# Optimization experiments

Measured on AMD Instinct MI355X. Metric: run time of the kernel, lower is better.

Reference implementation:

```python
import jax, jax.numpy as jnp
import numpy as np

B = 4096        # batch_size
D = 256         # feature_dim
N = 9000000     # dataset size (state buffer length)
G = 100         # num_groups
ALPHA = 0.5     # alpha_weight
GAMMA = 0.8
RHO = 8.0
LAM = 1.0       # lambada
ETA_P = 0.01
EPS = 1e-14
CLIP = 5.0


def setup_inputs() -> dict:
    key = jax.random.key(0)
    k = jax.random.split(key, 6)
    zis = jax.random.normal(k[0], (B, D), jnp.float32)
    zjs = jax.random.normal(k[1], (B, D), jnp.float32)
    # per-sample learned temperatures, small positive values
    taus_I = 0.01 + 0.2 * jax.random.uniform(k[2], (N,), jnp.float32)
    taus_T = 0.01 + 0.2 * jax.random.uniform(k[3], (N,), jnp.float32)
    group_info_I = jax.random.randint(k[4], (N,), 0, G, dtype=jnp.int32)
    group_info_T = jax.random.randint(k[5], (N,), 0, G, dtype=jnp.int32)
    ids = jnp.arange(B, dtype=jnp.int32)  # unique sample indices
    zeros_N = jnp.zeros((N,), jnp.float32)
    return {
        "zis": zis, "zjs": zjs,
        "s_I": zeros_N, "s_T": zeros_N, "b_I": zeros_N, "b_T": zeros_N,
        "z_I": jnp.zeros((G,), jnp.float32), "z_T": jnp.zeros((G,), jnp.float32),
        "p_I": jnp.ones((G,), jnp.float32) / G, "p_T": jnp.ones((G,), jnp.float32) / G,
        "taus_I": taus_I, "taus_T": taus_T,
        "ids": ids, "group_info_I": group_info_I, "group_info_T": group_info_T,
    }


def _l2norm(x):
    return x / jnp.maximum(jnp.linalg.norm(x, axis=1, keepdims=True), 1e-12)


def reference(zis, zjs, s_I, s_T, b_I, b_T, z_I, z_T, p_I, p_T,
              taus_I, taus_T, ids, group_info_I, group_info_T):
    zis = _l2norm(zis)
    zjs = _l2norm(zjs)
    sim = zis @ zjs.T                                   # [B, B]
    diag = jnp.diagonal(sim)                            # [B]
    mask_neg = 1.0 - jnp.eye(B, dtype=sim.dtype)
    image_diffs = sim - diag[:, None]
    text_diffs = sim - diag[None, :]

    tau_I = taus_I[ids]                                 # [B]
    tau_T = taus_T[ids]
    idt = jax.lax.stop_gradient(image_diffs / tau_I[:, None])
    tdt = jax.lax.stop_gradient(text_diffs / tau_T[None, :])

    # running max state (numerically-stable exp)
    old_b_I = b_I[ids]
    b_I_new = jnp.maximum(jnp.max(idt, axis=1), old_b_I)    # [B]
    old_b_T = b_T[ids]
    b_T_new = jnp.maximum(jnp.max(tdt, axis=0), old_b_T)    # [B]
    b_I = b_I.at[ids].set(b_I_new)
    b_T = b_T.at[ids].set(b_T_new)

    exp_I = jnp.exp(idt - b_I_new[:, None]) * mask_neg
    exp_T = jnp.exp(tdt - b_T_new[None, :]) * mask_neg
    g_I = jnp.sum(exp_I, axis=1)                         # [B]
    g_T = jnp.sum(exp_T, axis=0)                         # [B]

    # EMA of softmax denominators with max-rescaling
    s_I_new = (1.0 - GAMMA) * s_I[ids] * jnp.exp(old_b_I - b_I_new) + GAMMA * g_I
    s_T_new = (1.0 - GAMMA) * s_T[ids] * jnp.exp(old_b_T - b_T_new) + GAMMA * g_T
    s_I = s_I.at[ids].set(s_I_new)
    s_T = s_T.at[ids].set(s_T_new)
    s_I_c = jnp.maximum(s_I_new, EPS)
    s_T_c = jnp.maximum(s_T_new, EPS)

    w_I = exp_I / s_I_c[:, None]
    w_T = exp_T / s_T_c[None, :]

    gid_I = group_info_I[ids]                            # [B]
    gid_T = group_info_T[ids]
    gw_I = G * p_I[gid_I]                                # [B]
    gw_T = G * p_T[gid_T]

    image_loss = jnp.sum(w_I * gw_I[:, None] * image_diffs, axis=1)   # [B]
    text_loss = jnp.sum(w_T * gw_T[None, :] * text_diffs, axis=0)     # [B]
    total_loss = ALPHA * image_loss.mean() + (1.0 - ALPHA) * text_loss.mean()

    # per-group adversarial weight update
    F_I = tau_I * (jnp.log(s_I_c) + b_I_new + RHO)       # [B]
    F_T = tau_T * (jnp.log(s_T_c) + b_T_new + RHO)
    ones_b = jnp.ones((B,), sim.dtype)
    cnt_I = jnp.maximum(jax.ops.segment_sum(ones_b, gid_I, num_segments=G), 1.0)
    cnt_T = jnp.maximum(jax.ops.segment_sum(ones_b, gid_T, num_segments=G), 1.0)
    grad_p_I = jax.ops.segment_sum(F_I, gid_I, num_segments=G) / cnt_I
    grad_p_T = jax.ops.segment_sum(F_T, gid_T, num_segments=G) / cnt_T

    z_I = (1.0 - GAMMA) * z_I + GAMMA * grad_p_I
    z_T = (1.0 - GAMMA) * z_T + GAMMA * grad_p_T
    grad_hp_I = -LAM * jnp.log(p_I + EPS) - LAM
    grad_hp_T = -LAM * jnp.log(p_T + EPS) - LAM
    new_p_I = p_I * jnp.exp(2.0 * ETA_P * jnp.clip(z_I + grad_hp_I, -CLIP, CLIP))
    new_p_T = p_T * jnp.exp(2.0 * ETA_P * jnp.clip(z_T + grad_hp_T, -CLIP, CLIP))
    p_I = new_p_I / new_p_I.sum()
    p_T = new_p_T / new_p_T.sum()

    return total_loss, p_I, p_T
```

## Files before the change

kernel.cpp:

```cpp
#include <hip/hip_runtime.h>
#include <hip/hip_bf16.h>
#include <math.h>

#define BB 4096
#define DD 256
#define GG 100
#define GAMMA_C 0.8f
#define RHO_C 8.0f
#define ALPHA_C 0.5f
#define EPS_C 1e-14f
#define NSR 64
#define NSC 128

typedef __bf16 bf16x8 __attribute__((ext_vector_type(8)));
typedef float f32x16 __attribute__((ext_vector_type(16)));

__device__ inline int swzLoc(int r31, int k) {
    return ((k >> 4) << 9) | (((((k >> 3) & 1) << 5) | r31) << 3) | (k & 7);
}

__device__ inline float blockReduceSum(float v, float* lds) {
    for (int o = 32; o > 0; o >>= 1) v += __shfl_down(v, o);
    int lane = threadIdx.x & 63, wid = threadIdx.x >> 6;
    if (lane == 0) lds[wid] = v;
    __syncthreads();
    if (threadIdx.x == 0) {
        float r = lds[0];
        int nw = blockDim.x >> 6;
        for (int w = 1; w < nw; w++) r += lds[w];
        lds[0] = r;
    }
    __syncthreads();
    float r = lds[0];
    __syncthreads();
    return r;
}

__global__ void __launch_bounds__(256) norm_kernel(const float* __restrict__ zis,
                            const float* __restrict__ zjs,
                            ushort* __restrict__ zhi, ushort* __restrict__ zlo,
                            ushort* __restrict__ whi, ushort* __restrict__ wlo,
                            float* __restrict__ diag, float* __restrict__ acc) {
    __shared__ ushort st[4][8192];
    int rb = blockIdx.x;
    int wv = threadIdx.x >> 6, lane = threadIdx.x & 63;
    if (rb == 0) { acc[threadIdx.x] = 0.f; acc[threadIdx.x + 256] = 0.f; }
    for (int rr = 0; rr < 8; rr++) {
        int r = rb * 32 + wv * 8 + rr;
        float4 zv = *(const float4*)&zis[r * DD + lane * 4];
        float4 wv4 = *(const float4*)&zjs[r * DD + lane * 4];
        float sz = zv.x * zv.x + zv.y * zv.y + zv.z * zv.z + zv.w * zv.w;
        float sw = wv4.x * wv4.x + wv4.y * wv4.y + wv4.z * wv4.z + wv4.w * wv4.w;
        float dt = zv.x * wv4.x + zv.y * wv4.y + zv.z * wv4.z + zv.w * wv4.w;
        for (int mask = 1; mask <= 32; mask <<= 1) {
            sz += __shfl_xor(sz, mask);
            sw += __shfl_xor(sw, mask);
            dt += __shfl_xor(dt, mask);
        }
        float iz = 1.0f / fmaxf(sqrtf(sz), 1e-12f);
        float iw = 1.0f / fmaxf(sqrtf(sw), 1e-12f);
        if (lane == 0) diag[r] = dt * iz * iw;
        float nz[4] = {zv.x * iz, zv.y * iz, zv.z * iz, zv.w * iz};
        float nw[4] = {wv4.x * iw, wv4.y * iw, wv4.z * iw, wv4.w * iw};
        int r31 = wv * 8 + rr;
        for (int e = 0; e < 4; e++) {
            int k = lane * 4 + e;
            int li = swzLoc(r31, k);
            __hip_bfloat16 hz = __float2bfloat16(nz[e]);
            __hip_bfloat16 lz = __float2bfloat16(nz[e] - __bfloat162float(hz));
            __hip_bfloat16 hw = __float2bfloat16(nw[e]);
            __hip_bfloat16 lw = __float2bfloat16(nw[e] - __bfloat162float(hw));
            st[0][li] = *(ushort*)&hz;
            st[1][li] = *(ushort*)&lz;
            st[2][li] = *(ushort*)&hw;
            st[3][li] = *(ushort*)&lw;
        }
    }
    __syncthreads();
    size_t base = (size_t)rb * 8192;
    ushort* dsts[4] = {zhi + base, zlo + base, whi + base, wlo + base};
    for (int a = 0; a < 4; a++) {
        uint4* d = (uint4*)dsts[a];
        const uint4* s = (const uint4*)st[a];
        for (int it = 0; it < 4; it++) {
            int idx = it * 256 + threadIdx.x;
            d[idx] = s[idx];
        }
    }
}

__global__ void __launch_bounds__(256, 4) fused_tile(const ushort* __restrict__ Ahi,
        const ushort* __restrict__ Alo, const ushort* __restrict__ Bhi,
        const ushort* __restrict__ Blo, const float* __restrict__ diag,
        const float* __restrict__ tausI, const float* __restrict__ tausT,
        const int* __restrict__ ids,
        float* __restrict__ pmR, float* __restrict__ pgR, float* __restrict__ pwR,
        float* __restrict__ pmC, float* __restrict__ pgC, float* __restrict__ pwC) {
    __shared__ float rDiag[128], rITau[128];
    __shared__ float cDiag[64], cITau[64];

    int lane = threadIdx.x & 63;
    int wv = threadIdx.x >> 6;
    int bm = blockIdx.y * 128, bn = blockIdx.x * 64;
    int h = lane >> 5, cl = lane & 31;

    if (threadIdx.x < 128) {
        int r = bm + threadIdx.x;
        rDiag[threadIdx.x] = diag[r];
        rITau[threadIdx.x] = 1.0f / tausI[ids[r]];
    } else if (threadIdx.x < 192) {
        int c = bn + threadIdx.x - 128;
        cDiag[threadIdx.x - 128] = diag[c];
        cITau[threadIdx.x - 128] = 1.0f / tausT[ids[c]];
    }

    int aBase = (blockIdx.y * 4 + wv) * 8192;
    int b0 = (blockIdx.x * 2) * 8192;
    int b1 = b0 + 8192;
    int lofs = lane * 8;

    f32x16 acc[2] = {};
    bf16x8 ah, al, bh0, bl0, bh1, bl1;
    ah  = *(const bf16x8*)&Ahi[aBase + lofs];
    al  = *(const bf16x8*)&Alo[aBase + lofs];
    bh0 = *(const bf16x8*)&Bhi[b0 + lofs];
    bl0 = *(const bf16x8*)&Blo[b0 + lofs];
    bh1 = *(const bf16x8*)&Bhi[b1 + lofs];
    bl1 = *(const bf16x8*)&Blo[b1 + lofs];
#pragma unroll
    for (int s = 0; s < 16; s++) {
        bf16x8 nah, nal, nbh0, nbl0, nbh1, nbl1;
        if (s < 15) {
            int so = (s + 1) * 512 + lofs;
            nah  = *(const bf16x8*)&Ahi[aBase + so];
            nal  = *(const bf16x8*)&Alo[aBase + so];
            nbh0 = *(const bf16x8*)&Bhi[b0 + so];
            nbl0 = *(const bf16x8*)&Blo[b0 + so];
            nbh1 = *(const bf16x8*)&Bhi[b1 + so];
            nbl1 = *(const bf16x8*)&Blo[b1 + so];
        }
        acc[0] = __builtin_amdgcn_mfma_f32_32x32x16_bf16(ah, bh0, acc[0], 0, 0, 0);
        acc[0] = __builtin_amdgcn_mfma_f32_32x32x16_bf16(ah, bl0, acc[0], 0, 0, 0);
        acc[0] = __builtin_amdgcn_mfma_f32_32x32x16_bf16(al, bh0, acc[0], 0, 0, 0);
        acc[1] = __builtin_amdgcn_mfma_f32_32x32x16_bf16(ah, bh1, acc[1], 0, 0, 0);
        acc[1] = __builtin_amdgcn_mfma_f32_32x32x16_bf16(ah, bl1, acc[1], 0, 0, 0);
        acc[1] = __builtin_amdgcn_mfma_f32_32x32x16_bf16(al, bh1, acc[1], 0, 0, 0);
        ah = nah; al = nal; bh0 = nbh0; bl0 = nbl0; bh1 = nbh1; bl1 = nbl1;
    }
    __syncthreads();

    float cd2[2], cit2[2], cbloc[2], cg[2] = {}, cw[2] = {};
    for (int u = 0; u < 2; u++) {
        int clc = u * 32 + cl;
        cd2[u] = cDiag[clc];
        cit2[u] = cITau[clc];
        float m = -INFINITY;
        for (int reg = 0; reg < 16; reg++) m = fmaxf(m, acc[u][reg]);
        m = fmaxf(m, __shfl_xor(m, 32));
        cbloc[u] = (m - cd2[u]) * cit2[u];
    }
    for (int u = 0; u < 2; u++) {
        int gc = bn + u * 32 + cl;
        for (int reg = 0; reg < 16; reg++) {
            int gr = bm + wv * 32 + (reg & 3) + 4 * h + 8 * (reg >> 2);
            float v = acc[u][reg];
            bool off = gr != gc;
            float dvT = v - cd2[u];
            float eT = off ? __expf(dvT * cit2[u] - cbloc[u]) : 0.f;
            cg[u] += eT;
            cw[u] += eT * dvT;
        }
    }
    int stripeC = blockIdx.y * 4 + wv;
    for (int u = 0; u < 2; u++) {
        cg[u] += __shfl_xor(cg[u], 32);
        cw[u] += __shfl_xor(cw[u], 32);
        if (h == 0) {
            size_t o = (size_t)stripeC * BB + bn + u * 32 + cl;
            pmC[o] = cbloc[u];
            pgC[o] = cg[u];
            pwC[o] = cw[u];
        }
    }

    int stripeR = blockIdx.x;
    for (int q = 0; q < 4; q++) {
        float rd4[4], rit4[4], bloc[4], rg[4] = {}, rw[4] = {};
        for (int j = 0; j < 4; j++) {
            int rl = wv * 32 + 8 * q + 4 * h + j;
            rd4[j] = rDiag[rl];
            rit4[j] = rITau[rl];
        }
        for (int j = 0; j < 4; j++) {
            float m = fmaxf(acc[0][4 * q + j], acc[1][4 * q + j]);
            for (int mask = 1; mask <= 16; mask <<= 1)
                m = fmaxf(m, __shfl_xor(m, mask));
            bloc[j] = (m - rd4[j]) * rit4[j];
        }
        for (int u = 0; u < 2; u++) {
            int gc = bn + u * 32 + cl;
            for (int j = 0; j < 4; j++) {
                int gr = bm + wv * 32 + 8 * q + 4 * h + j;
                float v = acc[u][4 * q + j];
                bool off = gr != gc;
                float dvI = v - rd4[j];
                float eI = off ? __expf(dvI * rit4[j] - bloc[j]) : 0.f;
                rg[j] += eI;
                rw[j] += eI * dvI;
            }
        }
        for (int j = 0; j < 4; j++)
            for (int mask = 1; mask <= 16; mask <<= 1) {
                rg[j] += __shfl_xor(rg[j], mask);
                rw[j] += __shfl_xor(rw[j], mask);
            }
        if (cl == 0) {
            size_t o = (size_t)stripeR * BB + bm + wv * 32 + 8 * q + 4 * h;
            *(float4*)&pmR[o] = make_float4(bloc[0], bloc[1], bloc[2], bloc[3]);
            *(float4*)&pgR[o] = make_float4(rg[0], rg[1], rg[2], rg[3]);
            *(float4*)&pwR[o] = make_float4(rw[0], rw[1], rw[2], rw[3]);
        }
    }
}

__global__ void __launch_bounds__(256) fin_kernel(
        const float* __restrict__ pmR, const float* __restrict__ pgR,
        const float* __restrict__ pwR, const float* __restrict__ pmC,
        const float* __restrict__ pgC, const float* __restrict__ pwC,
        const float* __restrict__ sI, const float* __restrict__ bI,
        const float* __restrict__ tausI, const int* __restrict__ gInfI,
        const float* __restrict__ pI,
        const float* __restrict__ sT, const float* __restrict__ bT,
        const float* __restrict__ tausT, const int* __restrict__ gInfT,
        const float* __restrict__ pT,
        const int* __restrict__ ids, float* __restrict__ acc,
        const float* __restrict__ zI, const float* __restrict__ zT,
        float* __restrict__ out) {
    __shared__ float lds[8];
    __shared__ float binF[GG], binC[GG];
    __shared__ int lastFlag;
    if (threadIdx.x < GG) { binF[threadIdx.x] = 0.f; binC[threadIdx.x] = 0.f; }
    __syncthreads();
    int side = blockIdx.x >> 4;
    int i = (blockIdx.x & 15) * 256 + threadIdx.x;
    int ns = side ? NSC : NSR;
    const float* pm = side ? pmC : pmR;
    const float* pg = side ? pgC : pgR;
    const float* pw = side ? pwC : pwR;
    const float* sS = side ? sT : sI;
    const float* bS = side ? bT : bI;
    const float* taus = side ? tausT : tausI;
    const int* ginfo = side ? gInfT : gInfI;
    const float* pP = side ? pT : pI;

    int id = ids[i];
    float oldb = bS[id];
    float m = -INFINITY;
    for (int s = 0; s < ns; s++) m = fmaxf(m, pm[(size_t)s * BB + i]);
    float bfin = fmaxf(m, oldb);
    float g = 0.f, wsum = 0.f;
    for (int s = 0; s < ns; s++) {
        float f = __expf(pm[(size_t)s * BB + i] - bfin);
        g += pg[(size_t)s * BB + i] * f;
        wsum += pw[(size_t)s * BB + i] * f;
    }
    float tau = taus[id];
    float snew = (1.f - GAMMA_C) * sS[id] * expf(oldb - bfin) + GAMMA_C * g;
    float sc = fmaxf(snew, EPS_C);
    int gid = ginfo[id];
    float gw = (float)GG * pP[gid];
    float loss = gw * wsum / sc;
    float F = tau * (logf(sc) + bfin + RHO_C);
    atomicAdd(&binF[gid], F);
    atomicAdd(&binC[gid], 1.0f);
    float lsum = blockReduceSum(loss, lds);
    if (threadIdx.x == 0) atomicAdd(&acc[side], lsum);
    __syncthreads();
    if (threadIdx.x < GG) {
        atomicAdd(&acc[2 + side * 200 + threadIdx.x], binF[threadIdx.x]);
        atomicAdd(&acc[102 + side * 200 + threadIdx.x], binC[threadIdx.x]);
    }

    __threadfence();
    if (threadIdx.x == 0) {
        int old = atomicAdd((int*)&acc[408], 1);
        lastFlag = (old == 31);
    }
    __syncthreads();
    if (!lastFlag) return;

    int gg = threadIdx.x;
    float npI = 0.f, npT = 0.f;
    if (gg < GG) {
        float cI = __hip_atomic_load(&acc[102 + gg], __ATOMIC_RELAXED, __HIP_MEMORY_SCOPE_AGENT);
        float fI = __hip_atomic_load(&acc[2 + gg], __ATOMIC_RELAXED, __HIP_MEMORY_SCOPE_AGENT);
        float gpI = fI / fmaxf(cI, 1.f);
        float zi = (1.f - GAMMA_C) * zI[gg] + GAMMA_C * gpI;
        float ghpI = -logf(pI[gg] + EPS_C) - 1.f;
        float ti = fminf(fmaxf(zi + ghpI, -5.f), 5.f);
        npI = pI[gg] * expf(0.02f * ti);

        float cT = __hip_atomic_load(&acc[302 + gg], __ATOMIC_RELAXED, __HIP_MEMORY_SCOPE_AGENT);
        float fT = __hip_atomic_load(&acc[202 + gg], __ATOMIC_RELAXED, __HIP_MEMORY_SCOPE_AGENT);
        float gpT = fT / fmaxf(cT, 1.f);
        float zt = (1.f - GAMMA_C) * zT[gg] + GAMMA_C * gpT;
        float ghpT = -logf(pT[gg] + EPS_C) - 1.f;
        float tt = fminf(fmaxf(zt + ghpT, -5.f), 5.f);
        npT = pT[gg] * expf(0.02f * tt);
    }
    float sumI = blockReduceSum(npI, lds);
    float sumT = blockReduceSum(npT, lds);
    if (gg < GG) {
        out[1 + gg] = npI / sumI;
        out[101 + gg] = npT / sumT;
    }
    if (gg == 0) {
        float lI = __hip_atomic_load(&acc[0], __ATOMIC_RELAXED, __HIP_MEMORY_SCOPE_AGENT);
        float lT = __hip_atomic_load(&acc[1], __ATOMIC_RELAXED, __HIP_MEMORY_SCOPE_AGENT);
        out[0] = ALPHA_C * (lI / (float)BB) + (1.f - ALPHA_C) * (lT / (float)BB);
    }
}

extern "C" void kernel_launch(void* const* d_in, const int* in_sizes, int n_in,
                              void* d_out, int out_size, void* d_ws, size_t ws_size,
                              hipStream_t stream) {
    const float* zis   = (const float*)d_in[0];
    const float* zjs   = (const float*)d_in[1];
    const float* s_I   = (const float*)d_in[2];
    const float* s_T   = (const float*)d_in[3];
    const float* b_I   = (const float*)d_in[4];
    const float* b_T   = (const float*)d_in[5];
    const float* z_I   = (const float*)d_in[6];
    const float* z_T   = (const float*)d_in[7];
    const float* p_I   = (const float*)d_in[8];
    const float* p_T   = (const float*)d_in[9];
    const float* tausI = (const float*)d_in[10];
    const float* tausT = (const float*)d_in[11];
    const int*   ids   = (const int*)d_in[12];
    const int*   gInfI = (const int*)d_in[13];
    const int*   gInfT = (const int*)d_in[14];
    float* out = (float*)d_out;

    char* ws = (char*)d_ws;
    ushort* zhi = (ushort*)ws;
    ushort* zlo = zhi + (size_t)BB * DD;
    ushort* whi = zlo + (size_t)BB * DD;
    ushort* wlo = whi + (size_t)BB * DD;
    float* acc  = (float*)(wlo + (size_t)BB * DD);
    float* diag = acc + 512;
    float* pmR  = diag + BB;
    float* pgR  = pmR + (size_t)NSR * BB;
    float* pwR  = pgR + (size_t)NSR * BB;
    float* pmC  = pwR + (size_t)NSR * BB;
    float* pgC  = pmC + (size_t)NSC * BB;
    float* pwC  = pgC + (size_t)NSC * BB;

    norm_kernel<<<128, 256, 0, stream>>>(zis, zjs, zhi, zlo, whi, wlo, diag, acc);
    fused_tile<<<dim3(64, 32), 256, 0, stream>>>(zhi, zlo, whi, wlo, diag,
            tausI, tausT, ids, pmR, pgR, pwR, pmC, pgC, pwC);
    fin_kernel<<<32, 256, 0, stream>>>(pmR, pgR, pwR, pmC, pgC, pwC,
            s_I, b_I, tausI, gInfI, p_I, s_T, b_T, tausT, gInfT, p_T, ids, acc,
            z_I, z_T, out);
}
```

Measured before the change: 325.1 us.

## Merge column partials in-block and parallelize final reduction across more blocks

The tile kernel now merges its four per-wave column partials (max, exp-sum, weighted sum) through shared memory before writing, which cuts the column-side partial buffer from 128 stripes to 32. The finalize kernel is relaunched with 128 blocks, each splitting the stripe loop over four thread groups with an online log-sum-exp merge, followed by a shared-memory combine. Both changes target the latency of the serial 64/128-iteration reduction done by only 32 blocks. In exchange the tile kernel gains an extra __syncthreads and some shared-memory use, which could affect occupancy.

Result: faster. 279.5 us (-14.0%).

```diff
diff --git a/kernel.cpp b/kernel.cpp
--- a/kernel.cpp
+++ b/kernel.cpp
@@ -10,7 +10,7 @@
 #define ALPHA_C 0.5f
 #define EPS_C 1e-14f
 #define NSR 64
-#define NSC 128
+#define NSC 32
 
 typedef __bf16 bf16x8 __attribute__((ext_vector_type(8)));
 typedef float f32x16 __attribute__((ext_vector_type(16)));
@@ -98,6 +98,7 @@
         float* __restrict__ pmC, float* __restrict__ pgC, float* __restrict__ pwC) {
     __shared__ float rDiag[128], rITau[128];
     __shared__ float cDiag[64], cITau[64];
+    __shared__ float cmS[4][64], cgS[4][64], cwS[4][64];
 
     int lane = threadIdx.x & 63;
     int wv = threadIdx.x >> 6;
@@ -171,16 +172,29 @@
             cw[u] += eT * dvT;
         }
     }
-    int stripeC = blockIdx.y * 4 + wv;
     for (int u = 0; u < 2; u++) {
         cg[u] += __shfl_xor(cg[u], 32);
         cw[u] += __shfl_xor(cw[u], 32);
         if (h == 0) {
-            size_t o = (size_t)stripeC * BB + bn + u * 32 + cl;
-            pmC[o] = cbloc[u];
-            pgC[o] = cg[u];
-            pwC[o] = cw[u];
-        }
+            cmS[wv][u * 32 + cl] = cbloc[u];
+            cgS[wv][u * 32 + cl] = cg[u];
+            cwS[wv][u * 32 + cl] = cw[u];
+        }
+    }
+    __syncthreads();
+    if (threadIdx.x < 64) {
+        int c = threadIdx.x;
+        float m = fmaxf(fmaxf(cmS[0][c], cmS[1][c]), fmaxf(cmS[2][c], cmS[3][c]));
+        float g = 0.f, w = 0.f;
+        for (int wq = 0; wq < 4; wq++) {
+            float f = __expf(cmS[wq][c] - m);
+            g += cgS[wq][c] * f;
+            w += cwS[wq][c] * f;
+        }
+        size_t o = (size_t)blockIdx.y * BB + bn + c;
+        pmC[o] = m;
+        pgC[o] = g;
+        pwC[o] = w;
     }
 
     int stripeR = blockIdx.x;
@@ -238,11 +252,14 @@
         float* __restrict__ out) {
     __shared__ float lds[8];
     __shared__ float binF[GG], binC[GG];
+    __shared__ float mS[4][64], gS[4][64], wS[4][64];
     __shared__ int lastFlag;
     if (threadIdx.x < GG) { binF[threadIdx.x] = 0.f; binC[threadIdx.x] = 0.f; }
-    __syncthreads();
-    int side = blockIdx.x >> 4;
-    int i = (blockIdx.x & 15) * 256 + threadIdx.x;
+    int side = blockIdx.x >> 6;
+    int chunk = blockIdx.x & 63;
+    int il = threadIdx.x & 63;
+    int sg = threadIdx.x >> 6;
+    int i = chunk * 64 + il;
     int ns = side ? NSC : NSR;
     const float* pm = side ? pmC : pmR;
     const float* pg = side ? pgC : pgR;
@@ -253,26 +270,45 @@
     const int* ginfo = side ? gInfT : gInfI;
     const float* pP = side ? pT : pI;
 
-    int id = ids[i];
-    float oldb = bS[id];
-    float m = -INFINITY;
-    for (int s = 0; s < ns; s++) m = fmaxf(m, pm[(size_t)s * BB + i]);
-    float bfin = fmaxf(m, oldb);
-    float g = 0.f, wsum = 0.f;
-    for (int s = 0; s < ns; s++) {
-        float f = __expf(pm[(size_t)s * BB + i] - bfin);
-        g += pg[(size_t)s * BB + i] * f;
-        wsum += pw[(size_t)s * BB + i] * f;
-    }
-    float tau = taus[id];
-    float snew = (1.f - GAMMA_C) * sS[id] * expf(oldb - bfin) + GAMMA_C * g;
-    float sc = fmaxf(snew, EPS_C);
-    int gid = ginfo[id];
-    float gw = (float)GG * pP[gid];
-    float loss = gw * wsum / sc;
-    float F = tau * (logf(sc) + bfin + RHO_C);
-    atomicAdd(&binF[gid], F);
-    atomicAdd(&binC[gid], 1.0f);
+    float m = -INFINITY, g = 0.f, w = 0.f;
+    for (int s = sg; s < ns; s += 4) {
+        float pms = pm[(size_t)s * BB + i];
+        float pgs = pg[(size_t)s * BB + i];
+        float pws = pw[(size_t)s * BB + i];
+        float mn = fmaxf(m, pms);
+        float fo = __expf(m - mn);
+        float fs = __expf(pms - mn);
+        g = g * fo + pgs * fs;
+        w = w * fo + pws * fs;
+        m = mn;
+    }
+    mS[sg][il] = m;
+    gS[sg][il] = g;
+    wS[sg][il] = w;
+    __syncthreads();
+
+    float loss = 0.f;
+    if (sg == 0) {
+        int id = ids[i];
+        float oldb = bS[id];
+        float mm = fmaxf(fmaxf(mS[0][il], mS[1][il]), fmaxf(mS[2][il], mS[3][il]));
+        float bfin = fmaxf(mm, oldb);
+        float gg2 = 0.f, ww2 = 0.f;
+        for (int q = 0; q < 4; q++) {
+            float f = __expf(mS[q][il] - bfin);
+            gg2 += gS[q][il] * f;
+            ww2 += wS[q][il] * f;
+        }
+        float tau = taus[id];
+        float snew = (1.f - GAMMA_C) * sS[id] * expf(oldb - bfin) + GAMMA_C * gg2;
+        float sc = fmaxf(snew, EPS_C);
+        int gid = ginfo[id];
+        float gw = (float)GG * pP[gid];
+        loss = gw * ww2 / sc;
+        float F = tau * (logf(sc) + bfin + RHO_C);
+        atomicAdd(&binF[gid], F);
+        atomicAdd(&binC[gid], 1.0f);
+    }
     float lsum = blockReduceSum(loss, lds);
     if (threadIdx.x == 0) atomicAdd(&acc[side], lsum);
     __syncthreads();
@@ -284,7 +320,7 @@
     __threadfence();
     if (threadIdx.x == 0) {
         int old = atomicAdd((int*)&acc[408], 1);
-        lastFlag = (old == 31);
+        lastFlag = (old == 127);
     }
     __syncthreads();
     if (!lastFlag) return;
@@ -358,7 +394,7 @@
     norm_kernel<<<128, 256, 0, stream>>>(zis, zjs, zhi, zlo, whi, wlo, diag, acc);
     fused_tile<<<dim3(64, 32), 256, 0, stream>>>(zhi, zlo, whi, wlo, diag,
             tausI, tausT, ids, pmR, pgR, pwR, pmC, pgC, pwC);
-    fin_kernel<<<32, 256, 0, stream>>>(pmR, pgR, pwR, pmC, pgC, pwC,
+    fin_kernel<<<128, 256, 0, stream>>>(pmR, pgR, pwR, pmC, pgC, pwC,
             s_I, b_I, tausI, gInfI, p_I, s_T, b_T, tausT, gInfT, p_T, ids, acc,
             z_I, z_T, out);
 }
```
